# Kernel optimization log

Measured on AMD Instinct MI355X. Metric: run time of the kernel, lower is better.

## Reference

```python
import jax, jax.numpy as jnp
import numpy as np

EPS_OT = 0.05
SINK_ITERS = 3
HEADS = 8


def _l2norm(x, axis):
    n = jnp.sqrt(jnp.sum(x * x, axis=axis, keepdims=True))
    return x / jnp.maximum(n, 1e-12)


def _conv(x, w, b, pad):
    y = jax.lax.conv_general_dilated(x, w, (1, 1), [(pad, pad), (pad, pad)],
                                     dimension_numbers=('NCHW', 'OIHW', 'NCHW'))
    return y + b[None, :, None, None]


def _bn(x, g, b):
    # BatchNorm2d in training mode: batch statistics over (B,H,W)
    m = jnp.mean(x, axis=(0, 2, 3), keepdims=True)
    v = jnp.var(x, axis=(0, 2, 3), keepdims=True)
    return (x - m) / jnp.sqrt(v + 1e-5) * g[None, :, None, None] + b[None, :, None, None]


def setup_inputs() -> dict:
    key = jax.random.key(0)
    ks = jax.random.split(key, 16)
    B, C, H, W = 2, 256, 64, 64
    TXT = 512
    rn = lambda k, shp, s=0.02: jax.random.normal(k, shp, dtype=jnp.float32) * s
    return {
        'img_feat': jax.random.normal(ks[0], (B, C, H, W), jnp.float32),
        'txt_feat': jax.random.normal(ks[1], (B, TXT), jnp.float32),
        'density_map': jax.random.uniform(ks[2], (B, 1, H, W), dtype=jnp.float32),
        'tp_w': rn(ks[3], (C, TXT)), 'tp_b': jnp.zeros((C,), jnp.float32),
        'wq': rn(ks[4], (C, C)), 'bq': jnp.zeros((C,), jnp.float32),
        'wk': rn(ks[5], (C, C)), 'bk': jnp.zeros((C,), jnp.float32),
        'wv': rn(ks[6], (C, C)), 'bv': jnp.zeros((C,), jnp.float32),
        'wo': rn(ks[7], (C, C)), 'bo': jnp.zeros((C,), jnp.float32),
        'ln_g': jnp.ones((C,), jnp.float32), 'ln_b': jnp.zeros((C,), jnp.float32),
        'op_w': rn(ks[8], (C, C, 1, 1)), 'op_b': jnp.zeros((C,), jnp.float32),
        'hm1_w': rn(ks[9], (C // 2, C, 3, 3)), 'hm1_b': jnp.zeros((C // 2,), jnp.float32),
        'hm_bn_g': jnp.ones((C // 2,), jnp.float32), 'hm_bn_b': jnp.zeros((C // 2,), jnp.float32),
        'hm2_w': rn(ks[10], (2, C // 2, 1, 1)), 'hm2_b': jnp.zeros((2,), jnp.float32),
        'hv1_w': rn(ks[11], (C // 2, C, 3, 3)), 'hv1_b': jnp.zeros((C // 2,), jnp.float32),
        'hv_bn_g': jnp.ones((C // 2,), jnp.float32), 'hv_bn_b': jnp.zeros((C // 2,), jnp.float32),
        'hv2_w': rn(ks[12], (2, C // 2, 1, 1)), 'hv2_b': jnp.zeros((2,), jnp.float32),
        'temperature': jnp.ones((1,), jnp.float32) * 0.07,
    }


def reference(img_feat, txt_feat, density_map, tp_w, tp_b, wq, bq, wk, bk, wv, bv,
              wo, bo, ln_g, ln_b, op_w, op_b, hm1_w, hm1_b, hm_bn_g, hm_bn_b,
              hm2_w, hm2_b, hv1_w, hv1_b, hv_bn_g, hv_bn_b, hv2_w, hv2_b, temperature):
    B, C, H, W = img_feat.shape
    N = H * W
    dh = C // HEADS

    # text projection -> single token [B,1,C]
    txt_emb = (txt_feat @ tp_w.T + tp_b)[:, None, :]
    img_flat = img_feat.reshape(B, C, N).transpose(0, 2, 1)  # [B,N,C]

    # multihead cross-attention, kv length 1
    q = (img_flat @ wq.T + bq).reshape(B, N, HEADS, dh)
    k = (txt_emb @ wk.T + bk).reshape(B, 1, HEADS, dh)
    v = (txt_emb @ wv.T + bv).reshape(B, 1, HEADS, dh)
    scores = jnp.einsum('bnhd,bmhd->bhnm', q, k) / np.float32(np.sqrt(dh))
    w_attn = jax.nn.softmax(scores, axis=-1)
    attn_out = jnp.einsum('bhnm,bmhd->bnhd', w_attn, v).reshape(B, N, C) @ wo.T + bo

    # residual + layernorm
    x = img_flat + attn_out
    mu = jnp.mean(x, axis=-1, keepdims=True)
    var = jnp.var(x, axis=-1, keepdims=True)
    source = (x - mu) / jnp.sqrt(var + 1e-5) * ln_g + ln_b  # [B,N,C]
    mod_img = source.transpose(0, 2, 1).reshape(B, C, H, W)

    # target marginal from density map
    target = jax.nn.relu(density_map.reshape(B, N)) + 1e-6
    q_marg = target / jnp.sum(target, axis=1, keepdims=True)

    # source marginal from cosine similarity to text
    img_n = _l2norm(mod_img, 1)
    txt_n = _l2norm(txt_emb[:, 0, :], 1)  # [B,C]
    cos = jnp.einsum('bchw,bc->bhw', img_n, txt_n).reshape(B, N)
    temp = jnp.maximum(temperature, 0.01)
    p_marg = jax.nn.softmax(cos / temp, axis=1)

    # Sinkhorn OT over NxN cosine cost
    sn = _l2norm(source, 2)
    sim = jnp.einsum('bnc,bmc->bnm', sn, sn)
    K = jnp.exp(-(1.0 - sim) / EPS_OT)
    u = jnp.ones_like(p_marg)
    vv = jnp.ones_like(q_marg)
    for _ in range(SINK_ITERS):
        vv = q_marg / (jnp.einsum('bnm,bn->bm', K, u) + 1e-8)
        u = p_marg / (jnp.einsum('bnm,bm->bn', K, vv) + 1e-8)
    T = u[:, :, None] * K * vv[:, None, :]
    fused = jnp.einsum('bnm,bnc->bmc', T, source)  # T^T @ source

    fused_feat = fused.transpose(0, 2, 1).reshape(B, C, H, W)
    out_feat = img_feat + _conv(fused_feat, op_w, op_b, 0)

    hm = _conv(jax.nn.relu(_bn(_conv(out_feat, hm1_w, hm1_b, 1), hm_bn_g, hm_bn_b)), hm2_w, hm2_b, 0)
    hv = _conv(jax.nn.relu(_bn(_conv(out_feat, hv1_w, hv1_b, 1), hv_bn_g, hv_bn_b)), hv2_w, hv2_b, 0)
    return (out_feat, hm, hv)
```

## Files before the change

kernel.cpp:

```cpp
#include <hip/hip_runtime.h>

#define B_ 2
#define C_ 256
#define N_ 4096
#define TXT_ 512
#define CH_ 128
#define TN 32
#define KSPLIT 4
#define PXR 4224
#define PXPAD 96
#define PXTOT (PXR + 2 * PXPAD)
#define L2E 28.853900817779268f

typedef unsigned short u16;
typedef unsigned char u8;
typedef __attribute__((ext_vector_type(8))) short short8;
typedef __attribute__((ext_vector_type(4))) float f32x4;
typedef __attribute__((ext_vector_type(2))) float f32x2;

__device__ __forceinline__ float bf2f(u16 v){
  union { unsigned u; float f; } w; w.u = ((unsigned)v) << 16; return w.f;
}
__device__ __forceinline__ u16 f2bf(float f){
  union { float f; unsigned u; } w; w.f = f;
  unsigned r = w.u + 0x7fffu + ((w.u >> 16) & 1u);
  return (u16)(r >> 16);
}

#define MFMA_BF16(a,b,c) __builtin_amdgcn_mfma_f32_16x16x32_bf16(a,b,c,0,0,0)

__device__ __forceinline__ void stage_tile(const u16* __restrict__ g, int stride, u16* lds, int t)
{
  #pragma unroll
  for (int q = 0; q < 4; q++){
    int e = q * 256 + t;
    int row = e >> 3;
    int slot = e & 7;
    const u16* gp = g + (size_t)row * stride + ((slot ^ (row & 7)) << 3);
    u16* lp = lds + (size_t)e * 8;
    __builtin_amdgcn_global_load_lds((const __attribute__((address_space(1))) void*)gp,
                                     (__attribute__((address_space(3))) void*)lp, 16, 0, 0);
  }
}

__device__ __forceinline__ void stage_tile256_64(const u16* __restrict__ g, int stride, u16* lds, int t)
{
  #pragma unroll
  for (int q = 0; q < 2; q++){
    int e = q * 256 + t;
    int row = e >> 3;
    int slot = e & 7;
    const u16* gp = g + (size_t)row * stride + ((slot ^ (row & 7)) << 3);
    u16* lp = lds + (size_t)e * 8;
    __builtin_amdgcn_global_load_lds((const __attribute__((address_space(1))) void*)gp,
                                     (__attribute__((address_space(3))) void*)lp, 16, 0, 0);
  }
}

__device__ __forceinline__ void stage_tile512_256(const u16* __restrict__ g, int stride, u16* lds, int t)
{
  #pragma unroll
  for (int q = 0; q < 4; q++){
    int e = q * 512 + t;
    int row = e >> 3;
    int slot = e & 7;
    const u16* gp = g + (size_t)row * stride + ((slot ^ (row & 7)) << 3);
    u16* lp = lds + (size_t)e * 8;
    __builtin_amdgcn_global_load_lds((const __attribute__((address_space(1))) void*)gp,
                                     (__attribute__((address_space(3))) void*)lp, 16, 0, 0);
  }
}

__device__ __forceinline__ short8 frag_ld(const u16* lds, int row, int slot)
{
  return *(const short8*)(lds + row * 64 + ((slot ^ (row & 7)) << 3));
}

__global__ __launch_bounds__(256) void k_text1(
    const float* __restrict__ txt, const float* __restrict__ tpw,
    const float* __restrict__ tpb, float* __restrict__ te)
{
  int b = blockIdx.y;
  int ch = blockIdx.x * 4 + (threadIdx.x >> 6);
  int lane = threadIdx.x & 63;
  const float* tb = txt + (size_t)b * TXT_;
  const float* wr = tpw + (size_t)ch * TXT_;
  float4 a0 = *reinterpret_cast<const float4*>(wr + lane * 4);
  float4 a1 = *reinterpret_cast<const float4*>(wr + 256 + lane * 4);
  float4 b0 = *reinterpret_cast<const float4*>(tb + lane * 4);
  float4 b1 = *reinterpret_cast<const float4*>(tb + 256 + lane * 4);
  float s = a0.x * b0.x + a0.y * b0.y + a0.z * b0.z + a0.w * b0.w
          + a1.x * b1.x + a1.y * b1.y + a1.z * b1.z + a1.w * b1.w;
  for (int o = 32; o > 0; o >>= 1) s += __shfl_down(s, o);
  if (lane == 0) te[b * C_ + ch] = s + tpb[ch];
}

__global__ __launch_bounds__(1024) void k_text2(
    const float* __restrict__ te, const float* __restrict__ wv,
    const float* __restrict__ bv, const float* __restrict__ wo,
    const float* __restrict__ bo,
    float* __restrict__ attn_c, float* __restrict__ txt_n)
{
  int b = blockIdx.x, t = threadIdx.x;
  int w = t >> 6, lane = t & 63;
  __shared__ float te_s[C_], vs_s[C_];
  __shared__ float red[16];
  __shared__ float inv_s;
  if (t < C_) te_s[t] = te[b * C_ + t];
  __syncthreads();
  {
    float nv = (t < C_) ? te_s[t] * te_s[t] : 0.f;
    for (int o = 32; o > 0; o >>= 1) nv += __shfl_down(nv, o);
    if (lane == 0) red[w] = nv;
  }
  __syncthreads();
  if (t == 0){
    float S = 0.f;
    for (int q = 0; q < 16; q++) S += red[q];
    inv_s = 1.f / fmaxf(sqrtf(S), 1e-12f);
  }
  #pragma unroll
  for (int r = 0; r < 16; r++){
    int ch = r * 16 + w;
    float4 av = *reinterpret_cast<const float4*>(wv + (size_t)ch * C_ + lane * 4);
    float s = av.x * te_s[lane * 4] + av.y * te_s[lane * 4 + 1]
            + av.z * te_s[lane * 4 + 2] + av.w * te_s[lane * 4 + 3];
    for (int o = 32; o > 0; o >>= 1) s += __shfl_down(s, o);
    if (lane == 0) vs_s[ch] = s + bv[ch];
  }
  __syncthreads();
  #pragma unroll
  for (int r = 0; r < 16; r++){
    int ch = r * 16 + w;
    float4 av = *reinterpret_cast<const float4*>(wo + (size_t)ch * C_ + lane * 4);
    float s = av.x * vs_s[lane * 4] + av.y * vs_s[lane * 4 + 1]
            + av.z * vs_s[lane * 4 + 2] + av.w * vs_s[lane * 4 + 3];
    for (int o = 32; o > 0; o >>= 1) s += __shfl_down(s, o);
    if (lane == 0) attn_c[b * C_ + ch] = s + bo[ch];
  }
  if (t < C_) txt_n[b * C_ + t] = te_s[t] * inv_s;
}

__global__ __launch_bounds__(256) void k_source(
    const float* __restrict__ img, const float* __restrict__ attn_c,
    const float* __restrict__ ln_g, const float* __restrict__ ln_b,
    const float* __restrict__ txt_n,
    u16* __restrict__ srcT, u16* __restrict__ snb, float* __restrict__ cosv)
{
  int b = blockIdx.y;
  int n0 = blockIdx.x * TN;
  int t = threadIdx.x;
  __shared__ float x[C_][TN + 1];
  __shared__ float ps[8][TN];
  __shared__ float ps2[8][TN];
  __shared__ float ac_s[C_], g_s[C_], bb_s[C_], tn_s[C_];
  __shared__ float mean_s[TN], rstd_s[TN], rn_s[TN];
  ac_s[t] = attn_c[b * C_ + t];
  g_s[t]  = ln_g[t];
  bb_s[t] = ln_b[t];
  tn_s[t] = txt_n[b * C_ + t];
  const float* ib = img + (size_t)b * C_ * N_ + n0;
  for (int k = 0; k < TN; k++){
    int e = t + k * 256;
    int c = e >> 5, nn = e & 31;
    x[c][nn] = ib[(size_t)c * N_ + nn];
  }
  __syncthreads();
  for (int k = 0; k < TN; k++){
    int e = t + k * 256;
    int c = e >> 5, nn = e & 31;
    x[c][nn] += ac_s[c];
  }
  __syncthreads();
  {
    int p = t >> 5, nn = t & 31;
    float s1 = 0.f, s2 = 0.f;
    for (int j = 0; j < 32; j++){
      float v = x[p + 8 * j][nn];
      s1 += v; s2 += v * v;
    }
    ps[p][nn] = s1; ps2[p][nn] = s2;
  }
  __syncthreads();
  if (t < TN){
    float S1 = 0.f, S2 = 0.f;
    for (int pp = 0; pp < 8; pp++){ S1 += ps[pp][t]; S2 += ps2[pp][t]; }
    float mean = S1 * (1.f / C_);
    float var = S2 * (1.f / C_) - mean * mean;
    mean_s[t] = mean;
    rstd_s[t] = rsqrtf(var + 1e-5f);
  }
  __syncthreads();
  for (int k = 0; k < TN; k++){
    float sval = (x[t][k] - mean_s[k]) * rstd_s[k] * g_s[t] + bb_s[t];
    x[t][k] = sval;
  }
  for (int kq = 0; kq < TN; kq += 4){
    ushort4 pkv;
    pkv.x = f2bf(x[t][kq + 0]);
    pkv.y = f2bf(x[t][kq + 1]);
    pkv.z = f2bf(x[t][kq + 2]);
    pkv.w = f2bf(x[t][kq + 3]);
    *reinterpret_cast<ushort4*>(&srcT[(size_t)(b * C_ + t) * N_ + n0 + kq]) = pkv;
  }
  __syncthreads();
  {
    int p = t >> 5, nn = t & 31;
    float s2 = 0.f, sd = 0.f;
    for (int j = 0; j < 32; j++){
      int c = p + 8 * j;
      float v = x[c][nn];
      s2 += v * v; sd += v * tn_s[c];
    }
    ps[p][nn] = s2; ps2[p][nn] = sd;
  }
  __syncthreads();
  if (t < TN){
    float S2 = 0.f, SD = 0.f;
    for (int pp = 0; pp < 8; pp++){ S2 += ps[pp][t]; SD += ps2[pp][t]; }
    float nrm = sqrtf(S2);
    float rn = 1.f / fmaxf(nrm, 1e-12f);
    rn_s[t] = rn;
    cosv[(b << 12) + n0 + t] = SD * rn;
  }
  __syncthreads();
  for (int k = 0; k < TN; k++){
    snb[(size_t)((b << 12) + n0 + k) * C_ + t] = f2bf(x[t][k] * rn_s[k]);
  }
}

__global__ __launch_bounds__(256) void k_qmarg(const float* __restrict__ dens, float* __restrict__ q){
  int b = blockIdx.x, t = threadIdx.x;
  __shared__ float red[256];
  const float* d = dens + (size_t)b * N_;
  float s = 0.f;
  for (int n = t; n < N_; n += 256) s += fmaxf(d[n], 0.f) + 1e-6f;
  red[t] = s; __syncthreads();
  for (int o = 128; o > 0; o >>= 1){ if (t < o) red[t] += red[t + o]; __syncthreads(); }
  float inv = 1.f / red[0];
  for (int n = t; n < N_; n += 256) q[b * N_ + n] = (fmaxf(d[n], 0.f) + 1e-6f) * inv;
}

__global__ __launch_bounds__(256) void k_pmarg(const float* __restrict__ cosv,
    const float* __restrict__ temp_p, float* __restrict__ p){
  int b = blockIdx.x, t = threadIdx.x;
  __shared__ float red[256];
  float temp = fmaxf(temp_p[0], 0.01f);
  float inv_t = 1.f / temp;
  const float* cb = cosv + (size_t)b * N_;
  float m = -1e30f;
  for (int n = t; n < N_; n += 256) m = fmaxf(m, cb[n] * inv_t);
  red[t] = m; __syncthreads();
  for (int o = 128; o > 0; o >>= 1){ if (t < o) red[t] = fmaxf(red[t], red[t + o]); __syncthreads(); }
  m = red[0]; __syncthreads();
  float s = 0.f;
  for (int n = t; n < N_; n += 256) s += expf(cb[n] * inv_t - m);
  red[t] = s; __syncthreads();
  for (int o = 128; o > 0; o >>= 1){ if (t < o) red[t] += red[t + o]; __syncthreads(); }
  float invs = 1.f / red[0];
  for (int n = t; n < N_; n += 256) p[b * N_ + n] = expf(cb[n] * inv_t - m) * invs;
}

__global__ __launch_bounds__(256) void k_zero(float* __restrict__ p, int n){
  int i = blockIdx.x * 256 + threadIdx.x;
  if (i < n) p[i] = 0.f;
}

__global__ __launch_bounds__(256) void k_kgen(
    const u16* __restrict__ snb, u8* __restrict__ Kp, float* __restrict__ colsum)
{
  int b = blockIdx.z;
  int m0 = blockIdx.x << 7, n0 = blockIdx.y << 7;
  int t = threadIdx.x;
  int lane = t & 63, w = t >> 6;
  int wr = w >> 1, wc = w & 1;
  __shared__ __align__(16) u16 shbuf[128 * 128];
  u16* Al = shbuf;
  u16* Bl = shbuf + 128 * 64;
  __shared__ float cs[128];
  if (t < 128) cs[t] = 0.f;
  f32x4 zero = {0.f, 0.f, 0.f, 0.f};
  f32x4 acc[4][4];
  #pragma unroll
  for (int i = 0; i < 4; i++){
    #pragma unroll
    for (int j = 0; j < 4; j++) acc[i][j] = zero;
  }
  const u16* sb = snb + (size_t)b * N_ * C_;
  const u16* ga = sb + (size_t)m0 * C_;
  const u16* gb = sb + (size_t)n0 * C_;
  for (int kt = 0; kt < C_; kt += 64){
    stage_tile(ga + kt, C_, Al, t);
    stage_tile(gb + kt, C_, Bl, t);
    __syncthreads();
    #pragma unroll
    for (int kh = 0; kh < 2; kh++){
      short8 af[4], bfv[4];
      #pragma unroll
      for (int i = 0; i < 4; i++){
        af[i]  = frag_ld(Al, wr * 64 + i * 16 + (lane & 15), kh * 4 + (lane >> 4));
        bfv[i] = frag_ld(Bl, wc * 64 + i * 16 + (lane & 15), kh * 4 + (lane >> 4));
      }
      #pragma unroll
      for (int i = 0; i < 4; i++){
        #pragma unroll
        for (int j = 0; j < 4; j++)
          acc[i][j] = MFMA_BF16(af[i], bfv[j], acc[i][j]);
      }
    }
    __syncthreads();
  }
  u8* CtT = (u8*)shbuf;
  #pragma unroll
  for (int j = 0; j < 4; j++){
    int col = wc * 64 + j * 16 + (lane & 15);
    float csum = 0.f;
    #pragma unroll
    for (int i = 0; i < 4; i++){
      int rb = wr * 64 + i * 16 + (lane >> 4) * 4;
      float e0 = __builtin_amdgcn_exp2f(fmaf(acc[i][j][0], L2E, -L2E));
      float e1 = __builtin_amdgcn_exp2f(fmaf(acc[i][j][1], L2E, -L2E));
      float e2 = __builtin_amdgcn_exp2f(fmaf(acc[i][j][2], L2E, -L2E));
      float e3 = __builtin_amdgcn_exp2f(fmaf(acc[i][j][3], L2E, -L2E));
      int pk = __builtin_amdgcn_cvt_pk_fp8_f32(e0, e1, 0, false);
      pk = __builtin_amdgcn_cvt_pk_fp8_f32(e2, e3, pk, true);
      f32x2 d0 = __builtin_amdgcn_cvt_pk_f32_fp8(pk, false);
      f32x2 d1 = __builtin_amdgcn_cvt_pk_f32_fp8(pk, true);
      csum += (d0.x + d0.y) + (d1.x + d1.y);
      int wq = rb >> 2;
      *reinterpret_cast<unsigned*>(CtT + col * 128 + ((wq ^ ((col & 7) << 2)) << 2)) = (unsigned)pk;
    }
    atomicAdd(&cs[col], csum);
  }
  __syncthreads();
  u8* Kb = Kp + (size_t)b * N_ * N_;
  for (int e = t; e < 1024; e += 256){
    int row = e >> 3, un = e & 7;
    uint4 v = *(const uint4*)(CtT + row * 128 + ((un ^ (row & 7)) << 4));
    *reinterpret_cast<uint4*>(&Kb[(size_t)(n0 + row) * N_ + m0 + (un << 4)]) = v;
  }
  if (t < 128) atomicAdd(&colsum[b * N_ + n0 + t], cs[t]);
}

__global__ __launch_bounds__(256) void k_div(
    const float* __restrict__ marg, const float* __restrict__ denom, float* __restrict__ outp){
  int i = blockIdx.x * 256 + threadIdx.x;
  if (i < B_ * N_) outp[i] = marg[i] / (denom[i] + 1e-8f);
}

__global__ __launch_bounds__(256) void k_mv(
    const u8* __restrict__ Kp, const float* __restrict__ x,
    const float* __restrict__ marg, float* __restrict__ outp)
{
  int r0 = blockIdx.x * 8;
  int b = r0 >> 12;
  int t = threadIdx.x, w = t >> 6, lane = t & 63;
  __shared__ __align__(16) float xs[N_];
  const float* xb = x + b * N_;
  for (int i = t; i < N_ / 4; i += 256)
    reinterpret_cast<float4*>(xs)[i] = reinterpret_cast<const float4*>(xb)[i];
  __syncthreads();
  int r = r0 + w * 2;
  const u8* Kr0 = Kp + (size_t)b * N_ * N_ + (size_t)(r & (N_ - 1)) * N_;
  const u8* Kr1 = Kr0 + N_;
  float acc0 = 0.f, acc1 = 0.f;
  #pragma unroll
  for (int p = 0; p < 4; p++){
    int idx = p * 1024 + lane * 16;
    uint4 a = *reinterpret_cast<const uint4*>(Kr0 + idx);
    uint4 c = *reinterpret_cast<const uint4*>(Kr1 + idx);
    #pragma unroll
    for (int q = 0; q < 4; q++){
      unsigned aw = (q == 0) ? a.x : (q == 1) ? a.y : (q == 2) ? a.z : a.w;
      unsigned cw = (q == 0) ? c.x : (q == 1) ? c.y : (q == 2) ? c.z : c.w;
      float4 xv = *reinterpret_cast<const float4*>(xs + idx + q * 4);
      f32x2 al = __builtin_amdgcn_cvt_pk_f32_fp8((int)aw, false);
      f32x2 ah = __builtin_amdgcn_cvt_pk_f32_fp8((int)aw, true);
      f32x2 cl = __builtin_amdgcn_cvt_pk_f32_fp8((int)cw, false);
      f32x2 ch = __builtin_amdgcn_cvt_pk_f32_fp8((int)cw, true);
      acc0 += al.x * xv.x + al.y * xv.y + ah.x * xv.z + ah.y * xv.w;
      acc1 += cl.x * xv.x + cl.y * xv.y + ch.x * xv.z + ch.y * xv.w;
    }
  }
  for (int o = 32; o > 0; o >>= 1){
    acc0 += __shfl_down(acc0, o);
    acc1 += __shfl_down(acc1, o);
  }
  if (lane == 0){
    outp[r] = marg[r] / (acc0 + 1e-8f);
    outp[r + 1] = marg[r + 1] / (acc1 + 1e-8f);
  }
}

__global__ __launch_bounds__(256) void k_uscale(
    const u16* __restrict__ srcT, const float* __restrict__ uu, u16* __restrict__ usrcT)
{
  int i = blockIdx.x * 256 + threadIdx.x;
  int n8 = i & (N_ / 8 - 1);
  int row = i >> 9;
  int b = row >> 8;
  const u16* s = srcT + (size_t)row * N_ + n8 * 8;
  short8 v = *reinterpret_cast<const short8*>(s);
  const float* ub = uu + b * N_ + n8 * 8;
  short8 o;
  #pragma unroll
  for (int q = 0; q < 8; q++) o[q] = (short)f2bf(bf2f((u16)v[q]) * ub[q]);
  *reinterpret_cast<short8*>(usrcT + (size_t)row * N_ + n8 * 8) = o;
}

__global__ __launch_bounds__(512) void k_full(
    const u8* __restrict__ Kp, const u16* __restrict__ usrcT,
    const float* __restrict__ vvv,
    u16* __restrict__ p0, u16* __restrict__ p1,
    u16* __restrict__ p2, u16* __restrict__ p3)
{
  int m0 = blockIdx.x << 6;
  int b = blockIdx.z >> 2, ks = blockIdx.z & 3;
  int t = threadIdx.x, lane = t & 63, w = t >> 6;
  __shared__ __align__(16) u16 shbuf[64 * 64 + 256 * 64];
  __shared__ float vsm[64];
  u16* Al = shbuf;
  u16* Bl = shbuf + 64 * 64;
  if (t < 64) vsm[t] = vvv[b * N_ + m0 + t];
  f32x4 zero = {0.f, 0.f, 0.f, 0.f};
  f32x4 acc[4][2];
  #pragma unroll
  for (int i = 0; i < 4; i++){
    #pragma unroll
    for (int j = 0; j < 2; j++) acc[i][j] = zero;
  }
  const u8* ka = Kp + (size_t)b * N_ * N_ + (size_t)m0 * N_ + ks * (N_ / KSPLIT);
  const u16* ub = usrcT + (size_t)b * C_ * N_ + ks * (N_ / KSPLIT);
  for (int kt = 0; kt < N_ / KSPLIT; kt += 64){
    {
      int row = t >> 3, slot = t & 7;
      const u8* gp = ka + (size_t)row * N_ + kt + ((slot ^ (row & 7)) << 3);
      uint2 v8 = *reinterpret_cast<const uint2*>(gp);
      f32x2 q0 = __builtin_amdgcn_cvt_pk_f32_fp8((int)v8.x, false);
      f32x2 q1 = __builtin_amdgcn_cvt_pk_f32_fp8((int)v8.x, true);
      f32x2 q2 = __builtin_amdgcn_cvt_pk_f32_fp8((int)v8.y, false);
      f32x2 q3 = __builtin_amdgcn_cvt_pk_f32_fp8((int)v8.y, true);
      union { short8 s; unsigned u[4]; } o;
      asm("v_cvt_pk_bf16_f32 %0, %1, %2" : "=v"(o.u[0]) : "v"(q0.x), "v"(q0.y));
      asm("v_cvt_pk_bf16_f32 %0, %1, %2" : "=v"(o.u[1]) : "v"(q1.x), "v"(q1.y));
      asm("v_cvt_pk_bf16_f32 %0, %1, %2" : "=v"(o.u[2]) : "v"(q2.x), "v"(q2.y));
      asm("v_cvt_pk_bf16_f32 %0, %1, %2" : "=v"(o.u[3]) : "v"(q3.x), "v"(q3.y));
      *reinterpret_cast<short8*>(Al + (size_t)t * 8) = o.s;
    }
    stage_tile512_256(ub + kt, N_, Bl, t);
    __syncthreads();
    #pragma unroll
    for (int kh = 0; kh < 2; kh++){
      short8 af[4], bfv[2];
      #pragma unroll
      for (int i = 0; i < 4; i++)
        af[i] = frag_ld(Al, i * 16 + (lane & 15), kh * 4 + (lane >> 4));
      #pragma unroll
      for (int j = 0; j < 2; j++)
        bfv[j] = frag_ld(Bl, w * 32 + j * 16 + (lane & 15), kh * 4 + (lane >> 4));
      #pragma unroll
      for (int i = 0; i < 4; i++){
        #pragma unroll
        for (int j = 0; j < 2; j++)
          acc[i][j] = MFMA_BF16(af[i], bfv[j], acc[i][j]);
      }
    }
    __syncthreads();
  }
  u16* Ct = shbuf;
  #pragma unroll
  for (int j = 0; j < 2; j++){
    int col = w * 32 + j * 16 + (lane & 15);
    #pragma unroll
    for (int i = 0; i < 4; i++){
      int rb = i * 16 + (lane >> 4) * 4;
      #pragma unroll
      for (int r = 0; r < 4; r++){
        int row = rb + r;
        Ct[row * 256 + ((((col >> 3) ^ (row & 7)) << 3) | (col & 7))] =
            f2bf(acc[i][j][r] * vsm[row]);
      }
    }
  }
  __syncthreads();
  u16* P = (ks == 0) ? p0 : (ks == 1) ? p1 : (ks == 2) ? p2 : p3;
  for (int e = t; e < 2048; e += 512){
    int row = e >> 5, un = e & 31;
    short8 v8 = *(const short8*)(Ct + row * 256 + ((un ^ (row & 7)) << 3));
    *reinterpret_cast<short8*>(&P[(size_t)((b << 12) + m0 + row) * C_ + (un << 3)]) = v8;
  }
}

__global__ __launch_bounds__(256) void k_wcast(const float* __restrict__ w, u16* __restrict__ o){
  int i = blockIdx.x * 256 + threadIdx.x;
  o[i] = f2bf(w[i]);
}

__global__ __launch_bounds__(256) void k_opconv(
    const u16* __restrict__ opwB, const float* __restrict__ opb,
    const u16* __restrict__ p0, const u16* __restrict__ p1,
    const u16* __restrict__ p2, const u16* __restrict__ p3,
    const float* __restrict__ img, float* __restrict__ outf)
{
  int b = blockIdx.z;
  int n0 = blockIdx.x << 6;
  int co0 = blockIdx.y << 7;
  int t = threadIdx.x, lane = t & 63, w = t >> 6;
  int wr = w >> 1, wc = w & 1;
  __shared__ __align__(16) u16 Al[128 * 64];
  __shared__ __align__(16) u16 Bl[64 * 64];
  f32x4 zero = {0.f, 0.f, 0.f, 0.f};
  f32x4 acc[4][2];
  #pragma unroll
  for (int i = 0; i < 4; i++){
    #pragma unroll
    for (int j = 0; j < 2; j++) acc[i][j] = zero;
  }
  for (int ct = 0; ct < C_; ct += 64){
    stage_tile(opwB + (size_t)co0 * C_ + ct, C_, Al, t);
    #pragma unroll
    for (int q = 0; q < 2; q++){
      int e = q * 256 + t;
      int row = e >> 3, slot = e & 7;
      int col = ct + ((slot ^ (row & 7)) << 3);
      size_t idx = (size_t)((b << 12) + n0 + row) * C_ + col;
      short8 a0 = *reinterpret_cast<const short8*>(p0 + idx);
      short8 a1 = *reinterpret_cast<const short8*>(p1 + idx);
      short8 a2 = *reinterpret_cast<const short8*>(p2 + idx);
      short8 a3 = *reinterpret_cast<const short8*>(p3 + idx);
      short8 o;
      #pragma unroll
      for (int k = 0; k < 8; k++)
        o[k] = (short)f2bf(bf2f((u16)a0[k]) + bf2f((u16)a1[k]) + bf2f((u16)a2[k]) + bf2f((u16)a3[k]));
      *reinterpret_cast<short8*>(Bl + (size_t)e * 8) = o;
    }
    __syncthreads();
    #pragma unroll
    for (int kh = 0; kh < 2; kh++){
      short8 af[4], bfv[2];
      #pragma unroll
      for (int i = 0; i < 4; i++)
        af[i] = frag_ld(Al, wr * 64 + i * 16 + (lane & 15), kh * 4 + (lane >> 4));
      #pragma unroll
      for (int j = 0; j < 2; j++)
        bfv[j] = frag_ld(Bl, wc * 32 + j * 16 + (lane & 15), kh * 4 + (lane >> 4));
      #pragma unroll
      for (int i = 0; i < 4; i++){
        #pragma unroll
        for (int j = 0; j < 2; j++)
          acc[i][j] = MFMA_BF16(af[i], bfv[j], acc[i][j]);
      }
    }
    __syncthreads();
  }
  #pragma unroll
  for (int i = 0; i < 4; i++){
    int cb = co0 + wr * 64 + i * 16 + (lane >> 4) * 4;
    #pragma unroll
    for (int j = 0; j < 2; j++){
      int nc = n0 + wc * 32 + j * 16 + (lane & 15);
      #pragma unroll
      for (int r = 0; r < 4; r++){
        int co = cb + r;
        size_t oi = (size_t)(b * C_ + co) * N_ + nc;
        outf[oi] = acc[i][j][r] + img[oi] + opb[co];
      }
    }
  }
}

__global__ __launch_bounds__(256) void k_tr(const float* __restrict__ outf, u16* __restrict__ inTp)
{
  int b = blockIdx.z;
  int c0 = blockIdx.y << 6;
  int px0 = blockIdx.x << 6;
  int t = threadIdx.x;
  __shared__ float tile[64][65];
  int tx = t & 63, ty4 = t >> 6;
  for (int cc = ty4; cc < 64; cc += 4)
    tile[cc][tx] = outf[((size_t)(b * C_) + c0 + cc) * N_ + px0 + tx];
  __syncthreads();
  int p = t >> 2, cg = (t & 3) << 4;
  int px = px0 + p;
  int y = px >> 6, x = px & 63;
  int pxp = y * 66 + x + 1;
  u16* dst = inTp + ((size_t)b * PXTOT + PXPAD + pxp) * C_ + c0 + cg;
  #pragma unroll
  for (int q = 0; q < 16; q += 4){
    ushort4 pk;
    pk.x = f2bf(tile[cg + q + 0][p]);
    pk.y = f2bf(tile[cg + q + 1][p]);
    pk.z = f2bf(tile[cg + q + 2][p]);
    pk.w = f2bf(tile[cg + q + 3][p]);
    *reinterpret_cast<ushort4*>(dst + q) = pk;
  }
}

__global__ __launch_bounds__(256) void k_wtr(
    const float* __restrict__ hm1_w, const float* __restrict__ hv1_w,
    const float* __restrict__ hm1_b, const float* __restrict__ hv1_b,
    u16* __restrict__ Wt, float* __restrict__ biasF)
{
  int i = blockIdx.x * 256 + threadIdx.x;
  int ci = i & 255, co = (i >> 8) & 255, tap = i >> 16;
  float v = (co < CH_) ? hm1_w[((size_t)co * C_ + ci) * 9 + tap]
                       : hv1_w[((size_t)(co - CH_) * C_ + ci) * 9 + tap];
  Wt[i] = f2bf(v);
  if (i < CH_) biasF[i] = hm1_b[i];
  else if (i < 2 * CH_) biasF[i] = hv1_b[i - CH_];
}

__global__ __launch_bounds__(256) void k_conv3m(
    const u16* __restrict__ inTp, const u16* __restrict__ Wt,
    const float* __restrict__ biasF,
    u16* __restrict__ q0, u16* __restrict__ q1,
    u16* __restrict__ q2, u16* __restrict__ q3)
{
  int px0 = blockIdx.x << 6;
  int cot = blockIdx.y;
  int b = blockIdx.z >> 2, ks = blockIdx.z & 3;
  int t = threadIdx.x, lane = t & 63, w = t >> 6;
  int wr = w >> 1, wc = w & 1;
  __shared__ __align__(16) u16 Al[128 * 64];
  __shared__ __align__(16) u16 Bl[64 * 64];
  f32x4 zero = {0.f, 0.f, 0.f, 0.f};
  f32x4 acc[4][2];
  #pragma unroll
  for (int i = 0; i < 4; i++){
    #pragma unroll
    for (int j = 0; j < 2; j++) acc[i][j] = zero;
  }
  const u16* inb = inTp + ((size_t)b * PXTOT + PXPAD + px0) * C_;
  for (int s = ks * 9; s < ks * 9 + 9; s++){
    int tap = s >> 2, cic = (s & 3) << 6;
    int ky = tap / 3, kx = tap - ky * 3;
    int off = (ky - 1) * 66 + (kx - 1);
    stage_tile(Wt + ((size_t)tap * 256 + cot * 128) * C_ + cic, C_, Al, t);
    stage_tile256_64(inb + (ptrdiff_t)off * C_ + cic, C_, Bl, t);
    __syncthreads();
    #pragma unroll
    for (int kh = 0; kh < 2; kh++){
      short8 af[4], bfv[2];
      #pragma unroll
      for (int i = 0; i < 4; i++)
        af[i] = frag_ld(Al, wr * 64 + i * 16 + (lane & 15), kh * 4 + (lane >> 4));
      #pragma unroll
      for (int j = 0; j < 2; j++)
        bfv[j] = frag_ld(Bl, wc * 32 + j * 16 + (lane & 15), kh * 4 + (lane >> 4));
      #pragma unroll
      for (int i = 0; i < 4; i++){
        #pragma unroll
        for (int j = 0; j < 2; j++)
          acc[i][j] = MFMA_BF16(af[i], bfv[j], acc[i][j]);
      }
    }
    __syncthreads();
  }
  u16* P = (ks == 0) ? q0 : (ks == 1) ? q1 : (ks == 2) ? q2 : q3;
  #pragma unroll
  for (int i = 0; i < 4; i++){
    #pragma unroll
    for (int j = 0; j < 2; j++){
      int pxp = px0 + wc * 32 + j * 16 + (lane & 15);
      int y = pxp / 66;
      int xm = pxp - y * 66;
      bool valid = (xm >= 1 && xm <= 64);
      int outn = y * 64 + xm - 1;
      #pragma unroll
      for (int r = 0; r < 4; r++){
        int co = cot * 128 + wr * 64 + i * 16 + (lane >> 4) * 4 + r;
        if (valid){
          float bco = (ks == 0) ? biasF[co] : 0.f;
          P[((size_t)(b * 256 + co)) * N_ + outn] = f2bf(acc[i][j][r] + bco);
        }
      }
    }
  }
}

__global__ __launch_bounds__(256) void k_bnstats2(
    const u16* __restrict__ p0, const u16* __restrict__ p1,
    const u16* __restrict__ p2, const u16* __restrict__ p3,
    float* __restrict__ stats)
{
  int ch = blockIdx.x, t = threadIdx.x;
  __shared__ float r1[256], r2[256];
  float s1 = 0.f, s2 = 0.f;
  for (int i = t; i < B_ * N_; i += 256){
    int b = i >> 12, n = i & (N_ - 1);
    size_t idx = ((size_t)(b * 256 + ch)) * N_ + n;
    float v = bf2f(p0[idx]) + bf2f(p1[idx]) + bf2f(p2[idx]) + bf2f(p3[idx]);
    s1 += v; s2 += v * v;
  }
  r1[t] = s1; r2[t] = s2; __syncthreads();
  for (int o = 128; o > 0; o >>= 1){
    if (t < o){ r1[t] += r1[t + o]; r2[t] += r2[t + o]; }
    __syncthreads();
  }
  if (t == 0){
    float mean = r1[0] / (float)(B_ * N_);
    float var = r2[0] / (float)(B_ * N_) - mean * mean;
    stats[ch * 2] = mean;
    stats[ch * 2 + 1] = rsqrtf(var + 1e-5f);
  }
}

__global__ __launch_bounds__(256) void k_headF(
    const u16* __restrict__ p0, const u16* __restrict__ p1,
    const u16* __restrict__ p2, const u16* __restrict__ p3,
    const float* __restrict__ stats,
    const float* __restrict__ hm_g, const float* __restrict__ hm_b,
    const float* __restrict__ hm2_w, const float* __restrict__ hm2_b,
    const float* __restrict__ hv_g, const float* __restrict__ hv_b,
    const float* __restrict__ hv2_w, const float* __restrict__ hv2_b,
    float* __restrict__ outhm, float* __restrict__ outhv)
{
  int t = threadIdx.x;
  int nl = t & 31, g = t >> 5;
  int idx0 = blockIdx.x * 32;
  int idx = idx0 + nl;
  int b = idx >> 12, n = idx & (N_ - 1);
  int head = g >> 2;
  int ch0 = (g & 3) * 32;
  const float* gg = head ? hv_g : hm_g;
  const float* gb = head ? hv_b : hm_b;
  const float* w2 = head ? hv2_w : hm2_w;
  float a0 = 0.f, a1 = 0.f;
  #pragma unroll 8
  for (int cc = 0; cc < 32; cc++){
    int ch = ch0 + cc;
    int fc = head * CH_ + ch;
    size_t id = ((size_t)(b * 256 + fc)) * N_ + n;
    float v = bf2f(p0[id]) + bf2f(p1[id]) + bf2f(p2[id]) + bf2f(p3[id]);
    float rr = fmaxf((v - stats[fc * 2]) * stats[fc * 2 + 1] * gg[ch] + gb[ch], 0.f);
    a0 += w2[ch] * rr;
    a1 += w2[CH_ + ch] * rr;
  }
  __shared__ float r0[8][32], r1[8][32];
  r0[g][nl] = a0; r1[g][nl] = a1;
  __syncthreads();
  if (t < 64){
    int hh = t >> 5, n2 = t & 31;
    int base = hh * 4;
    float s0 = r0[base][n2] + r0[base + 1][n2] + r0[base + 2][n2] + r0[base + 3][n2];
    float s1 = r1[base][n2] + r1[base + 1][n2] + r1[base + 2][n2] + r1[base + 3][n2];
    int idx2 = idx0 + n2;
    int b2 = idx2 >> 12, nn = idx2 & (N_ - 1);
    float* op = hh ? outhv : outhm;
    const float* bp = hh ? hv2_b : hm2_b;
    op[(size_t)(b2 * 2) * N_ + nn] = s0 + bp[0];
    op[(size_t)(b2 * 2 + 1) * N_ + nn] = s1 + bp[1];
  }
}

extern "C" void kernel_launch(void* const* d_in, const int* in_sizes, int n_in,
                              void* d_out, int out_size, void* d_ws, size_t ws_size,
                              hipStream_t stream)
{
  const float* img   = (const float*)d_in[0];
  const float* txt   = (const float*)d_in[1];
  const float* dens  = (const float*)d_in[2];
  const float* tp_w  = (const float*)d_in[3];
  const float* tp_b  = (const float*)d_in[4];
  const float* wv    = (const float*)d_in[9];
  const float* bv    = (const float*)d_in[10];
  const float* wo    = (const float*)d_in[11];
  const float* bo    = (const float*)d_in[12];
  const float* ln_g  = (const float*)d_in[13];
  const float* ln_b  = (const float*)d_in[14];
  const float* op_w  = (const float*)d_in[15];
  const float* op_b  = (const float*)d_in[16];
  const float* hm1_w = (const float*)d_in[17];
  const float* hm1_b = (const float*)d_in[18];
  const float* hm_g  = (const float*)d_in[19];
  const float* hm_b  = (const float*)d_in[20];
  const float* hm2_w = (const float*)d_in[21];
  const float* hm2_b = (const float*)d_in[22];
  const float* hv1_w = (const float*)d_in[23];
  const float* hv1_b = (const float*)d_in[24];
  const float* hv_g  = (const float*)d_in[25];
  const float* hv_b  = (const float*)d_in[26];
  const float* hv2_w = (const float*)d_in[27];
  const float* hv2_b = (const float*)d_in[28];
  const float* temp  = (const float*)d_in[29];

  char* wsb = (char*)d_ws;
  size_t off = 0;
  auto alloc = [&](size_t bytes) -> void* {
    void* p = wsb + off;
    off += (bytes + 255) & ~(size_t)255;
    return p;
  };
  u8*    Km     = (u8*)   alloc((size_t)B_ * N_ * N_ * sizeof(u8));
  u16*   snb16  = (u16*)  alloc((size_t)B_ * N_ * C_ * sizeof(u16));
  u16*   srcT16 = (u16*)  alloc((size_t)B_ * C_ * N_ * sizeof(u16));
  u16*   usrcT  = (u16*)  alloc((size_t)B_ * C_ * N_ * sizeof(u16));
  u16*   part1  = (u16*)  alloc((size_t)B_ * N_ * C_ * sizeof(u16));
  u16*   part2  = (u16*)  alloc((size_t)B_ * N_ * C_ * sizeof(u16));
  u16*   part3  = (u16*)  alloc((size_t)B_ * N_ * C_ * sizeof(u16));
  u16*   inTp   = (u16*)  alloc((size_t)B_ * PXTOT * C_ * sizeof(u16));
  u16*   Wt     = (u16*)  alloc((size_t)9 * 256 * C_ * sizeof(u16));
  u16*   opwB   = (u16*)  alloc((size_t)C_ * C_ * sizeof(u16));
  float* biasF  = (float*)alloc(256 * sizeof(float));
  float* teb    = (float*)alloc(B_ * C_ * sizeof(float));
  float* attn_c = (float*)alloc(B_ * C_ * sizeof(float));
  float* txt_n  = (float*)alloc(B_ * C_ * sizeof(float));
  float* cosv   = (float*)alloc(B_ * N_ * sizeof(float));
  float* qm     = (float*)alloc(B_ * N_ * sizeof(float));
  float* pm     = (float*)alloc(B_ * N_ * sizeof(float));
  float* uu     = (float*)alloc(B_ * N_ * sizeof(float));
  float* vvv    = (float*)alloc(B_ * N_ * sizeof(float));
  float* colsum = (float*)alloc(B_ * N_ * sizeof(float));
  float* stats  = (float*)alloc(256 * 2 * sizeof(float));

  u16* part0 = snb16;

  float* outf  = (float*)d_out;
  float* outhm = outf + (size_t)B_ * C_ * N_;
  float* outhv = outhm + (size_t)B_ * 2 * N_;

  k_text1<<<dim3(64, B_), 256, 0, stream>>>(txt, tp_w, tp_b, teb);
  k_text2<<<B_, 1024, 0, stream>>>(teb, wv, bv, wo, bo, attn_c, txt_n);
  k_source<<<dim3(N_ / TN, B_), 256, 0, stream>>>(img, attn_c, ln_g, ln_b, txt_n, srcT16, snb16, cosv);
  k_qmarg<<<B_, 256, 0, stream>>>(dens, qm);
  k_pmarg<<<B_, 256, 0, stream>>>(cosv, temp, pm);
  k_zero<<<(B_ * N_ + 255) / 256, 256, 0, stream>>>(colsum, B_ * N_);
  k_wtr<<<9 * 256, 256, 0, stream>>>(hm1_w, hv1_w, hm1_b, hv1_b, Wt, biasF);
  k_wcast<<<C_ * C_ / 256, 256, 0, stream>>>(op_w, opwB);
  k_zero<<<((int)((size_t)B_ * PXTOT * C_ / 2) + 255) / 256, 256, 0, stream>>>((float*)inTp, (int)((size_t)B_ * PXTOT * C_ / 2));
  k_kgen<<<dim3(N_ / 128, N_ / 128, B_), 256, 0, stream>>>(snb16, Km, colsum);
  k_div<<<(B_ * N_ + 255) / 256, 256, 0, stream>>>(qm, colsum, vvv);
  k_mv<<<B_ * N_ / 8, 256, 0, stream>>>(Km, vvv, pm, uu);
  k_mv<<<B_ * N_ / 8, 256, 0, stream>>>(Km, uu, qm, vvv);
  k_mv<<<B_ * N_ / 8, 256, 0, stream>>>(Km, vvv, pm, uu);
  k_mv<<<B_ * N_ / 8, 256, 0, stream>>>(Km, uu, qm, vvv);
  k_mv<<<B_ * N_ / 8, 256, 0, stream>>>(Km, vvv, pm, uu);
  k_uscale<<<(B_ * C_ * N_ / 8 + 255) / 256, 256, 0, stream>>>(srcT16, uu, usrcT);
  k_full<<<dim3(N_ / 64, 1, B_ * KSPLIT), 512, 0, stream>>>(Km, usrcT, vvv, part0, part1, part2, part3);
  k_opconv<<<dim3(N_ / 64, C_ / 128, B_), 256, 0, stream>>>(opwB, op_b, part0, part1, part2, part3, img, outf);
  k_tr<<<dim3(N_ / 64, 4, B_), 256, 0, stream>>>(outf, inTp);
  k_conv3m<<<dim3(66, 2, B_ * KSPLIT), 256, 0, stream>>>(inTp, Wt, biasF, part0, part1, part2, part3);
  k_bnstats2<<<256, 256, 0, stream>>>(part0, part1, part2, part3, stats);
  k_headF<<<B_ * N_ / 32, 256, 0, stream>>>(part0, part1, part2, part3, stats,
      hm_g, hm_b, hm2_w, hm2_b, hv_g, hv_b, hv2_w, hv2_b, outhm, outhv);
}
```

Measured before the change: 230.2 us.

## Merge setup kernels, fuse div into first matvec, fold transpose into opconv

Combines the marginal, zeroing and weight-prep launches into two multi-role kernels, folds the v=q/colsum division into the first Sinkhorn matvec, and writes the bf16 padded transposed copy of out_feat directly from the opconv epilogue through a swizzled LDS tile instead of a separate transpose kernel. The matvec now handles four rows per wave with shared x loads from LDS. This aims to cut launch count, remove one full fp32 reread of out_feat, and reduce LDS traffic in the matvecs. It adds register pressure in opconv and matvec, and reuses the opconv A tile LDS buffer after the main loop.

```diff
diff --git a/kernel.cpp b/kernel.cpp
--- a/kernel.cpp
+++ b/kernel.cpp
@@ -229,41 +229,70 @@
   }
 }
 
-__global__ __launch_bounds__(256) void k_qmarg(const float* __restrict__ dens, float* __restrict__ q){
-  int b = blockIdx.x, t = threadIdx.x;
+__global__ __launch_bounds__(256) void k_marg(
+    const float* __restrict__ dens, const float* __restrict__ cosv,
+    const float* __restrict__ temp_p,
+    float* __restrict__ q, float* __restrict__ p, float* __restrict__ colsum)
+{
+  int bid = blockIdx.x, t = threadIdx.x;
   __shared__ float red[256];
-  const float* d = dens + (size_t)b * N_;
-  float s = 0.f;
-  for (int n = t; n < N_; n += 256) s += fmaxf(d[n], 0.f) + 1e-6f;
-  red[t] = s; __syncthreads();
-  for (int o = 128; o > 0; o >>= 1){ if (t < o) red[t] += red[t + o]; __syncthreads(); }
-  float inv = 1.f / red[0];
-  for (int n = t; n < N_; n += 256) q[b * N_ + n] = (fmaxf(d[n], 0.f) + 1e-6f) * inv;
-}
-
-__global__ __launch_bounds__(256) void k_pmarg(const float* __restrict__ cosv,
-    const float* __restrict__ temp_p, float* __restrict__ p){
-  int b = blockIdx.x, t = threadIdx.x;
-  __shared__ float red[256];
-  float temp = fmaxf(temp_p[0], 0.01f);
-  float inv_t = 1.f / temp;
-  const float* cb = cosv + (size_t)b * N_;
-  float m = -1e30f;
-  for (int n = t; n < N_; n += 256) m = fmaxf(m, cb[n] * inv_t);
-  red[t] = m; __syncthreads();
-  for (int o = 128; o > 0; o >>= 1){ if (t < o) red[t] = fmaxf(red[t], red[t + o]); __syncthreads(); }
-  m = red[0]; __syncthreads();
-  float s = 0.f;
-  for (int n = t; n < N_; n += 256) s += expf(cb[n] * inv_t - m);
-  red[t] = s; __syncthreads();
-  for (int o = 128; o > 0; o >>= 1){ if (t < o) red[t] += red[t + o]; __syncthreads(); }
-  float invs = 1.f / red[0];
-  for (int n = t; n < N_; n += 256) p[b * N_ + n] = expf(cb[n] * inv_t - m) * invs;
-}
-
-__global__ __launch_bounds__(256) void k_zero(float* __restrict__ p, int n){
-  int i = blockIdx.x * 256 + threadIdx.x;
-  if (i < n) p[i] = 0.f;
+  if (bid < B_){
+    int b = bid;
+    const float* d = dens + (size_t)b * N_;
+    float s = 0.f;
+    for (int n = t; n < N_; n += 256) s += fmaxf(d[n], 0.f) + 1e-6f;
+    red[t] = s; __syncthreads();
+    for (int o = 128; o > 0; o >>= 1){ if (t < o) red[t] += red[t + o]; __syncthreads(); }
+    float inv = 1.f / red[0];
+    for (int n = t; n < N_; n += 256) q[b * N_ + n] = (fmaxf(d[n], 0.f) + 1e-6f) * inv;
+  } else if (bid < 2 * B_){
+    int b = bid - B_;
+    float temp = fmaxf(temp_p[0], 0.01f);
+    float inv_t = 1.f / temp;
+    const float* cb = cosv + (size_t)b * N_;
+    float m = -1e30f;
+    for (int n = t; n < N_; n += 256) m = fmaxf(m, cb[n] * inv_t);
+    red[t] = m; __syncthreads();
+    for (int o = 128; o > 0; o >>= 1){ if (t < o) red[t] = fmaxf(red[t], red[t + o]); __syncthreads(); }
+    m = red[0]; __syncthreads();
+    float s = 0.f;
+    for (int n = t; n < N_; n += 256) s += expf(cb[n] * inv_t - m);
+    red[t] = s; __syncthreads();
+    for (int o = 128; o > 0; o >>= 1){ if (t < o) red[t] += red[t + o]; __syncthreads(); }
+    float invs = 1.f / red[0];
+    for (int n = t; n < N_; n += 256) p[b * N_ + n] = expf(cb[n] * inv_t - m) * invs;
+  } else {
+    int i = (bid - 2 * B_) * 256 + t;
+    if (i < B_ * N_) colsum[i] = 0.f;
+  }
+}
+
+__global__ __launch_bounds__(256) void k_prep(
+    const float* __restrict__ hm1_w, const float* __restrict__ hv1_w,
+    const float* __restrict__ hm1_b, const float* __restrict__ hv1_b,
+    const float* __restrict__ op_w,
+    u16* __restrict__ Wt, float* __restrict__ biasF,
+    u16* __restrict__ opwB, float* __restrict__ inTpf4)
+{
+  int bid = blockIdx.x, t = threadIdx.x;
+  if (bid < 2304){
+    int i = bid * 256 + t;
+    int ci = i & 255, co = (i >> 8) & 255, tap = i >> 16;
+    float v = (co < CH_) ? hm1_w[((size_t)co * C_ + ci) * 9 + tap]
+                         : hv1_w[((size_t)(co - CH_) * C_ + ci) * 9 + tap];
+    Wt[i] = f2bf(v);
+    if (i < CH_) biasF[i] = hm1_b[i];
+    else if (i < 2 * CH_) biasF[i] = hv1_b[i - CH_];
+  } else if (bid < 2560){
+    int i = (bid - 2304) * 256 + t;
+    opwB[i] = f2bf(op_w[i]);
+  } else {
+    int i = (bid - 2560) * 256 + t;
+    if (i < (int)((size_t)B_ * PXTOT * C_ * 2 / 16)){
+      float4 z = {0.f, 0.f, 0.f, 0.f};
+      reinterpret_cast<float4*>(inTpf4)[i] = z;
+    }
+  }
 }
 
 __global__ __launch_bounds__(256) void k_kgen(
@@ -342,53 +371,58 @@
   if (t < 128) atomicAdd(&colsum[b * N_ + n0 + t], cs[t]);
 }
 
-__global__ __launch_bounds__(256) void k_div(
-    const float* __restrict__ marg, const float* __restrict__ denom, float* __restrict__ outp){
-  int i = blockIdx.x * 256 + threadIdx.x;
-  if (i < B_ * N_) outp[i] = marg[i] / (denom[i] + 1e-8f);
-}
-
 __global__ __launch_bounds__(256) void k_mv(
     const u8* __restrict__ Kp, const float* __restrict__ x,
+    const float* __restrict__ denom,
     const float* __restrict__ marg, float* __restrict__ outp)
 {
-  int r0 = blockIdx.x * 8;
+  int r0 = blockIdx.x * 16;
   int b = r0 >> 12;
   int t = threadIdx.x, w = t >> 6, lane = t & 63;
   __shared__ __align__(16) float xs[N_];
   const float* xb = x + b * N_;
-  for (int i = t; i < N_ / 4; i += 256)
-    reinterpret_cast<float4*>(xs)[i] = reinterpret_cast<const float4*>(xb)[i];
-  __syncthreads();
-  int r = r0 + w * 2;
-  const u8* Kr0 = Kp + (size_t)b * N_ * N_ + (size_t)(r & (N_ - 1)) * N_;
-  const u8* Kr1 = Kr0 + N_;
-  float acc0 = 0.f, acc1 = 0.f;
+  if (denom){
+    const float* db = denom + b * N_;
+    for (int i = t; i < N_; i += 256) xs[i] = xb[i] / (db[i] + 1e-8f);
+  } else {
+    for (int i = t; i < N_ / 4; i += 256)
+      reinterpret_cast<float4*>(xs)[i] = reinterpret_cast<const float4*>(xb)[i];
+  }
+  __syncthreads();
+  int rbase = r0 + w * 4;
+  const u8* Kr = Kp + (size_t)b * N_ * N_ + (size_t)(rbase & (N_ - 1)) * N_;
+  float acc[4] = {0.f, 0.f, 0.f, 0.f};
   #pragma unroll
   for (int p = 0; p < 4; p++){
     int idx = p * 1024 + lane * 16;
-    uint4 a = *reinterpret_cast<const uint4*>(Kr0 + idx);
-    uint4 c = *reinterpret_cast<const uint4*>(Kr1 + idx);
-    #pragma unroll
-    for (int q = 0; q < 4; q++){
-      unsigned aw = (q == 0) ? a.x : (q == 1) ? a.y : (q == 2) ? a.z : a.w;
-      unsigned cw = (q == 0) ? c.x : (q == 1) ? c.y : (q == 2) ? c.z : c.w;
-      float4 xv = *reinterpret_cast<const float4*>(xs + idx + q * 4);
-      f32x2 al = __builtin_amdgcn_cvt_pk_f32_fp8((int)aw, false);
-      f32x2 ah = __builtin_amdgcn_cvt_pk_f32_fp8((int)aw, true);
-      f32x2 cl = __builtin_amdgcn_cvt_pk_f32_fp8((int)cw, false);
-      f32x2 ch = __builtin_amdgcn_cvt_pk_f32_fp8((int)cw, true);
-      acc0 += al.x * xv.x + al.y * xv.y + ah.x * xv.z + ah.y * xv.w;
-      acc1 += cl.x * xv.x + cl.y * xv.y + ch.x * xv.z + ch.y * xv.w;
-    }
-  }
-  for (int o = 32; o > 0; o >>= 1){
-    acc0 += __shfl_down(acc0, o);
-    acc1 += __shfl_down(acc1, o);
-  }
+    float4 xv0 = *reinterpret_cast<const float4*>(xs + idx);
+    float4 xv1 = *reinterpret_cast<const float4*>(xs + idx + 4);
+    float4 xv2 = *reinterpret_cast<const float4*>(xs + idx + 8);
+    float4 xv3 = *reinterpret_cast<const float4*>(xs + idx + 12);
+    #pragma unroll
+    for (int k = 0; k < 4; k++){
+      uint4 a = *reinterpret_cast<const uint4*>(Kr + (size_t)k * N_ + idx);
+      f32x2 l0 = __builtin_amdgcn_cvt_pk_f32_fp8((int)a.x, false);
+      f32x2 h0 = __builtin_amdgcn_cvt_pk_f32_fp8((int)a.x, true);
+      f32x2 l1 = __builtin_amdgcn_cvt_pk_f32_fp8((int)a.y, false);
+      f32x2 h1 = __builtin_amdgcn_cvt_pk_f32_fp8((int)a.y, true);
+      f32x2 l2 = __builtin_amdgcn_cvt_pk_f32_fp8((int)a.z, false);
+      f32x2 h2 = __builtin_amdgcn_cvt_pk_f32_fp8((int)a.z, true);
+      f32x2 l3 = __builtin_amdgcn_cvt_pk_f32_fp8((int)a.w, false);
+      f32x2 h3 = __builtin_amdgcn_cvt_pk_f32_fp8((int)a.w, true);
+      acc[k] += l0.x * xv0.x + l0.y * xv0.y + h0.x * xv0.z + h0.y * xv0.w
+              + l1.x * xv1.x + l1.y * xv1.y + h1.x * xv1.z + h1.y * xv1.w
+              + l2.x * xv2.x + l2.y * xv2.y + h2.x * xv2.z + h2.y * xv2.w
+              + l3.x * xv3.x + l3.y * xv3.y + h3.x * xv3.z + h3.y * xv3.w;
+    }
+  }
+  #pragma unroll
+  for (int k = 0; k < 4; k++)
+    for (int o = 32; o > 0; o >>= 1) acc[k] += __shfl_down(acc[k], o);
   if (lane == 0){
-    outp[r] = marg[r] / (acc0 + 1e-8f);
-    outp[r + 1] = marg[r + 1] / (acc1 + 1e-8f);
+    #pragma unroll
+    for (int k = 0; k < 4; k++)
+      outp[rbase + k] = marg[rbase + k] / (acc[k] + 1e-8f);
   }
 }
 
@@ -491,16 +525,12 @@
   }
 }
 
-__global__ __launch_bounds__(256) void k_wcast(const float* __restrict__ w, u16* __restrict__ o){
-  int i = blockIdx.x * 256 + threadIdx.x;
-  o[i] = f2bf(w[i]);
-}
-
 __global__ __launch_bounds__(256) void k_opconv(
     const u16* __restrict__ opwB, const float* __restrict__ opb,
     const u16* __restrict__ p0, const u16* __restrict__ p1,
     const u16* __restrict__ p2, const u16* __restrict__ p3,
-    const float* __restrict__ img, float* __restrict__ outf)
+    const float* __restrict__ img, float* __restrict__ outf,
+    u16* __restrict__ inTp)
 {
   int b = blockIdx.z;
   int n0 = blockIdx.x << 6;
@@ -553,6 +583,7 @@
     }
     __syncthreads();
   }
+  float fin[4][2][4];
   #pragma unroll
   for (int i = 0; i < 4; i++){
     int cb = co0 + wr * 64 + i * 16 + (lane >> 4) * 4;
@@ -563,51 +594,35 @@
       for (int r = 0; r < 4; r++){
         int co = cb + r;
         size_t oi = (size_t)(b * C_ + co) * N_ + nc;
-        outf[oi] = acc[i][j][r] + img[oi] + opb[co];
+        float v = acc[i][j][r] + img[oi] + opb[co];
+        outf[oi] = v;
+        fin[i][j][r] = v;
       }
     }
   }
-}
-
-__global__ __launch_bounds__(256) void k_tr(const float* __restrict__ outf, u16* __restrict__ inTp)
-{
-  int b = blockIdx.z;
-  int c0 = blockIdx.y << 6;
-  int px0 = blockIdx.x << 6;
-  int t = threadIdx.x;
-  __shared__ float tile[64][65];
-  int tx = t & 63, ty4 = t >> 6;
-  for (int cc = ty4; cc < 64; cc += 4)
-    tile[cc][tx] = outf[((size_t)(b * C_) + c0 + cc) * N_ + px0 + tx];
-  __syncthreads();
-  int p = t >> 2, cg = (t & 3) << 4;
-  int px = px0 + p;
-  int y = px >> 6, x = px & 63;
-  int pxp = y * 66 + x + 1;
-  u16* dst = inTp + ((size_t)b * PXTOT + PXPAD + pxp) * C_ + c0 + cg;
-  #pragma unroll
-  for (int q = 0; q < 16; q += 4){
-    ushort4 pk;
-    pk.x = f2bf(tile[cg + q + 0][p]);
-    pk.y = f2bf(tile[cg + q + 1][p]);
-    pk.z = f2bf(tile[cg + q + 2][p]);
-    pk.w = f2bf(tile[cg + q + 3][p]);
-    *reinterpret_cast<ushort4*>(dst + q) = pk;
-  }
-}
-
-__global__ __launch_bounds__(256) void k_wtr(
-    const float* __restrict__ hm1_w, const float* __restrict__ hv1_w,
-    const float* __restrict__ hm1_b, const float* __restrict__ hv1_b,
-    u16* __restrict__ Wt, float* __restrict__ biasF)
-{
-  int i = blockIdx.x * 256 + threadIdx.x;
-  int ci = i & 255, co = (i >> 8) & 255, tap = i >> 16;
-  float v = (co < CH_) ? hm1_w[((size_t)co * C_ + ci) * 9 + tap]
-                       : hv1_w[((size_t)(co - CH_) * C_ + ci) * 9 + tap];
-  Wt[i] = f2bf(v);
-  if (i < CH_) biasF[i] = hm1_b[i];
-  else if (i < 2 * CH_) biasF[i] = hv1_b[i - CH_];
+  u16* T = Al;
+  #pragma unroll
+  for (int i = 0; i < 4; i++){
+    int cb4 = wr * 64 + i * 16 + (lane >> 4) * 4;
+    #pragma unroll
+    for (int j = 0; j < 2; j++){
+      int ncL = wc * 32 + j * 16 + (lane & 15);
+      ushort4 pk;
+      pk.x = f2bf(fin[i][j][0]);
+      pk.y = f2bf(fin[i][j][1]);
+      pk.z = f2bf(fin[i][j][2]);
+      pk.w = f2bf(fin[i][j][3]);
+      *reinterpret_cast<ushort4*>(T + ncL * 128 + (cb4 ^ ((ncL & 15) << 3))) = pk;
+    }
+  }
+  __syncthreads();
+  int y = n0 >> 6;
+  for (int e = t; e < 1024; e += 256){
+    int px = e >> 4, u = e & 15;
+    uint4 v = *reinterpret_cast<const uint4*>(T + px * 128 + ((u << 3) ^ ((px & 15) << 3)));
+    int pxp = y * 66 + px + 1;
+    *reinterpret_cast<uint4*>(inTp + ((size_t)b * PXTOT + PXPAD + pxp) * C_ + co0 + u * 8) = v;
+  }
 }
 
 __global__ __launch_bounds__(256) void k_conv3m(
@@ -821,24 +836,18 @@
 
   k_text1<<<dim3(64, B_), 256, 0, stream>>>(txt, tp_w, tp_b, teb);
   k_text2<<<B_, 1024, 0, stream>>>(teb, wv, bv, wo, bo, attn_c, txt_n);
+  k_prep<<<2560 + 1104, 256, 0, stream>>>(hm1_w, hv1_w, hm1_b, hv1_b, op_w, Wt, biasF, opwB, (float*)inTp);
   k_source<<<dim3(N_ / TN, B_), 256, 0, stream>>>(img, attn_c, ln_g, ln_b, txt_n, srcT16, snb16, cosv);
-  k_qmarg<<<B_, 256, 0, stream>>>(dens, qm);
-  k_pmarg<<<B_, 256, 0, stream>>>(cosv, temp, pm);
-  k_zero<<<(B_ * N_ + 255) / 256, 256, 0, stream>>>(colsum, B_ * N_);
-  k_wtr<<<9 * 256, 256, 0, stream>>>(hm1_w, hv1_w, hm1_b, hv1_b, Wt, biasF);
-  k_wcast<<<C_ * C_ / 256, 256, 0, stream>>>(op_w, opwB);
-  k_zero<<<((int)((size_t)B_ * PXTOT * C_ / 2) + 255) / 256, 256, 0, stream>>>((float*)inTp, (int)((size_t)B_ * PXTOT * C_ / 2));
+  k_marg<<<2 * B_ + B_ * N_ / 256, 256, 0, stream>>>(dens, cosv, temp, qm, pm, colsum);
   k_kgen<<<dim3(N_ / 128, N_ / 128, B_), 256, 0, stream>>>(snb16, Km, colsum);
-  k_div<<<(B_ * N_ + 255) / 256, 256, 0, stream>>>(qm, colsum, vvv);
-  k_mv<<<B_ * N_ / 8, 256, 0, stream>>>(Km, vvv, pm, uu);
-  k_mv<<<B_ * N_ / 8, 256, 0, stream>>>(Km, uu, qm, vvv);
-  k_mv<<<B_ * N_ / 8, 256, 0, stream>>>(Km, vvv, pm, uu);
-  k_mv<<<B_ * N_ / 8, 256, 0, stream>>>(Km, uu, qm, vvv);
-  k_mv<<<B_ * N_ / 8, 256, 0, stream>>>(Km, vvv, pm, uu);
+  k_mv<<<B_ * N_ / 16, 256, 0, stream>>>(Km, qm, colsum, pm, uu);
+  k_mv<<<B_ * N_ / 16, 256, 0, stream>>>(Km, uu, nullptr, qm, vvv);
+  k_mv<<<B_ * N_ / 16, 256, 0, stream>>>(Km, vvv, nullptr, pm, uu);
+  k_mv<<<B_ * N_ / 16, 256, 0, stream>>>(Km, uu, nullptr, qm, vvv);
+  k_mv<<<B_ * N_ / 16, 256, 0, stream>>>(Km, vvv, nullptr, pm, uu);
   k_uscale<<<(B_ * C_ * N_ / 8 + 255) / 256, 256, 0, stream>>>(srcT16, uu, usrcT);
   k_full<<<dim3(N_ / 64, 1, B_ * KSPLIT), 512, 0, stream>>>(Km, usrcT, vvv, part0, part1, part2, part3);
-  k_opconv<<<dim3(N_ / 64, C_ / 128, B_), 256, 0, stream>>>(opwB, op_b, part0, part1, part2, part3, img, outf);
-  k_tr<<<dim3(N_ / 64, 4, B_), 256, 0, stream>>>(outf, inTp);
+  k_opconv<<<dim3(N_ / 64, C_ / 128, B_), 256, 0, stream>>>(opwB, op_b, part0, part1, part2, part3, img, outf, inTp);
   k_conv3m<<<dim3(66, 2, B_ * KSPLIT), 256, 0, stream>>>(inTp, Wt, biasF, part0, part1, part2, part3);
   k_bnstats2<<<256, 256, 0, stream>>>(part0, part1, part2, part3, stats);
   k_headF<<<B_ * N_ / 32, 256, 0, stream>>>(part0, part1, part2, part3, stats,
```

Measured after the change: 217.4 us. 1.06x faster.
